# Kernel tuning notes

Measured on AMD Instinct MI355X. Metric: run time of the kernel, lower is better.

## Reference

```python
import jax, jax.numpy as jnp
import numpy as np

TOPK = 4
EPS = 1e-8  # torch CosineSimilarity eps


def _retrieve(query, memory, k):
    # query: [B,S,D], memory: [N,S,D] -> [B,k,S,D]
    q = query.mean(axis=1)                      # [B,D]
    m = memory.mean(axis=1)                     # [N,D]
    qn = q / jnp.maximum(jnp.linalg.norm(q, axis=-1, keepdims=True), EPS)
    mn = m / jnp.maximum(jnp.linalg.norm(m, axis=-1, keepdims=True), EPS)
    sim = qn @ mn.T                             # [B,N] cosine similarity
    valid = (m.sum(axis=-1) != 0).astype(sim.dtype)[None, :]
    sim = sim * valid
    _, idx = jax.lax.top_k(sim, k)              # [B,k]
    return memory[idx]                          # gather -> [B,k,S,D]


def _generate(rem, ret, rem_w, rem_b, ret_w, ret_b, ew1, eb1, ew2, eb2):
    # rem: [B,S,D], ret: [B,K,S,D]; nn.Linear: y = x @ W.T + b
    r = rem @ rem_w.T + rem_b                   # [B,S,D]
    t = jnp.einsum('bksd,ed->bkse', ret, ret_w) + ret_b  # [B,K,S,D]
    score = jax.nn.softmax(
        jnp.einsum('bd,bkd->bk', r.mean(axis=1), t.mean(axis=2)), axis=1)  # [B,K]
    # stacked experts: Linear -> ReLU -> Linear per expert k
    h = jax.nn.relu(jnp.einsum('bksd,ked->bkse', ret, ew1) + eb1[None, :, None, :])
    eo = jnp.einsum('bkse,kfe->bksf', h, ew2) + eb2[None, :, None, :]  # [B,K,S,D]
    return jnp.einsum('bksd,bk->bsd', eo, score)


def setup_inputs() -> dict:
    key = jax.random.key(0)
    B, S, D, N, K = 64, 32, 512, 4096, TOPK
    ks = jax.random.split(key, 24)
    out = {
        'image': jax.random.normal(ks[0], (B, S, D), jnp.float32),
        'text': jax.random.normal(ks[1], (B, S, D), jnp.float32),
        'm1': jax.random.randint(ks[2], (B, 1), 0, 2).astype(jnp.int32),
        'm2': jax.random.randint(ks[3], (B, 1), 0, 2).astype(jnp.int32),
        'mem_image': jax.random.normal(ks[4], (N, S, D), jnp.float32),
        'mem_text': jax.random.normal(ks[5], (N, S, D), jnp.float32),
    }
    i = 6
    for pfx in ('img', 'txt'):
        out[f'{pfx}_rem_w'] = 0.02 * jax.random.normal(ks[i], (D, D), jnp.float32); i += 1
        out[f'{pfx}_rem_b'] = jnp.zeros((D,), jnp.float32)
        out[f'{pfx}_ret_w'] = 0.02 * jax.random.normal(ks[i], (D, D), jnp.float32); i += 1
        out[f'{pfx}_ret_b'] = jnp.zeros((D,), jnp.float32)
        out[f'{pfx}_ew1'] = 0.02 * jax.random.normal(ks[i], (K, D, D), jnp.float32); i += 1
        out[f'{pfx}_eb1'] = jnp.zeros((K, D), jnp.float32)
        out[f'{pfx}_ew2'] = 0.02 * jax.random.normal(ks[i], (K, D, D), jnp.float32); i += 1
        out[f'{pfx}_eb2'] = jnp.zeros((K, D), jnp.float32)
    return out


def reference(image, text, m1, m2, mem_image, mem_text,
              img_rem_w, img_rem_b, img_ret_w, img_ret_b, img_ew1, img_eb1, img_ew2, img_eb2,
              txt_rem_w, txt_rem_b, txt_ret_w, txt_ret_b, txt_ew1, txt_eb1, txt_ew2, txt_eb2):
    m1e = (m1 == 1)[:, 0]  # image exists
    m2e = (m2 == 1)[:, 0]  # text exists

    # generate missing image from existing text (compute full batch, mask after;
    # identical per-sample math to the subset computation in the original)
    ret_img = _retrieve(text, mem_image, TOPK)
    gen_img = _generate(text, ret_img, img_rem_w, img_rem_b, img_ret_w, img_ret_b,
                        img_ew1, img_eb1, img_ew2, img_eb2)
    gen_image_full = jnp.where(m2e[:, None, None], gen_img, 0.0)
    completed_image = jnp.where(jnp.logical_and(~m1e, m2e)[:, None, None], gen_img, image)

    # generate missing text from existing image
    ret_txt = _retrieve(image, mem_text, TOPK)
    gen_txt = _generate(image, ret_txt, txt_rem_w, txt_rem_b, txt_ret_w, txt_ret_b,
                        txt_ew1, txt_eb1, txt_ew2, txt_eb2)
    gen_text_full = jnp.where(m1e[:, None, None], gen_txt, 0.0)
    completed_text = jnp.where(jnp.logical_and(~m2e, m1e)[:, None, None], gen_txt, text)

    return (completed_image, completed_text, gen_image_full, gen_text_full)
```

## Files before the change

### kernel.cpp

```cpp
#include <hip/hip_runtime.h>
#include <hip/hip_fp16.h>

#define BB 64
#define SS 32
#define DD 512
#define NMEM 4096
#define KTOP 4
#define EPSV 1e-8f

typedef _Float16 f16;
typedef f16 f16x8 __attribute__((ext_vector_type(8)));
typedef f16 f16x4 __attribute__((ext_vector_type(4)));
typedef float f32x4 __attribute__((ext_vector_type(4)));

__global__ void k_wconv(const float* __restrict__ s0, const float* __restrict__ s1,
                        const float* __restrict__ s2, const float* __restrict__ s3,
                        f16* __restrict__ d0, f16* __restrict__ d1,
                        f16* __restrict__ d2, f16* __restrict__ d3) {
    const float* s; f16* d;
    switch (blockIdx.y) {
        case 0: s = s0; d = d0; break;
        case 1: s = s1; d = d1; break;
        case 2: s = s2; d = d2; break;
        default: s = s3; d = d3; break;
    }
    size_t i = ((size_t)blockIdx.x * 256 + threadIdx.x) * 4;
    float4 v = *(const float4*)(s + i);
    f16x4 o;
    o[0] = (f16)v.x; o[1] = (f16)v.y; o[2] = (f16)v.z; o[3] = (f16)v.w;
    *(f16x4*)(d + i) = o;
}

__global__ void k_qmean(const float* __restrict__ image, const float* __restrict__ text,
                        float* __restrict__ qmean, float* __restrict__ qn) {
    int mod = blockIdx.x >> 6;
    int b = blockIdx.x & 63;
    const float* q = (mod == 0) ? text : image;
    int t = threadIdx.x;
    const float* base = q + (size_t)b * SS * DD + t * 2;
    float ax = 0.f, ay = 0.f;
#pragma unroll
    for (int s = 0; s < SS; ++s) {
        float2 v = *(const float2*)(base + (size_t)s * DD);
        ax += v.x; ay += v.y;
    }
    ax *= (1.f / SS); ay *= (1.f / SS);
    float* qm = qmean + ((size_t)mod * BB + b) * DD;
    qm[t * 2] = ax; qm[t * 2 + 1] = ay;
    __shared__ float red[256];
    red[t] = ax * ax + ay * ay;
    __syncthreads();
    for (int off = 128; off > 0; off >>= 1) {
        if (t < off) red[t] += red[t + off];
        __syncthreads();
    }
    __shared__ float s_inv;
    if (t == 0) s_inv = 1.f / fmaxf(sqrtf(red[0]), EPSV);
    __syncthreads();
    float inv = s_inv;
    float* qo = qn + ((size_t)mod * BB + b) * DD;
    qo[t * 2] = ax * inv; qo[t * 2 + 1] = ay * inv;
}

__global__ void k_memmean_sim(const float* __restrict__ mem_image, const float* __restrict__ mem_text,
                              const float* __restrict__ qn, float* __restrict__ mmean,
                              float* __restrict__ sim) {
    int mod = blockIdx.x >> 12;
    int n = blockIdx.x & 4095;
    const float* mem = (mod == 0) ? mem_image : mem_text;
    int t = threadIdx.x;
    int cg = t & 127;
    int half = t >> 7;
    const float* base = mem + (size_t)n * SS * DD + (size_t)half * DD + cg * 4;
    float ax = 0.f, ay = 0.f, az = 0.f, aw = 0.f;
#pragma unroll
    for (int i = 0; i < SS / 2; ++i) {
        float4 v = *(const float4*)(base + (size_t)(i * 2) * DD);
        ax += v.x; ay += v.y; az += v.z; aw += v.w;
    }
    __shared__ float part[128][4];
    if (half) { part[cg][0] = ax; part[cg][1] = ay; part[cg][2] = az; part[cg][3] = aw; }
    __syncthreads();
    __shared__ float red[128], red2[128];
    __shared__ float smn[512];
    if (!half) {
        const float inv = 1.f / SS;
        ax = (ax + part[cg][0]) * inv;
        ay = (ay + part[cg][1]) * inv;
        az = (az + part[cg][2]) * inv;
        aw = (aw + part[cg][3]) * inv;
        float4 o; o.x = ax; o.y = ay; o.z = az; o.w = aw;
        *(float4*)(mmean + ((size_t)mod * NMEM + n) * DD + cg * 4) = o;
        red[cg] = ax * ax + ay * ay + az * az + aw * aw;
        red2[cg] = ax + ay + az + aw;
    }
    __syncthreads();
    for (int off = 64; off > 0; off >>= 1) {
        if (t < off) { red[t] += red[t + off]; red2[t] += red2[t + off]; }
        __syncthreads();
    }
    __shared__ float s_scale;
    if (t == 0) {
        float norm = sqrtf(red[0]);
        float valid = (red2[0] != 0.f) ? 1.f : 0.f;
        s_scale = valid / fmaxf(norm, EPSV);
    }
    __syncthreads();
    if (!half) {
        float sc = s_scale;
        smn[cg * 4] = ax * sc; smn[cg * 4 + 1] = ay * sc;
        smn[cg * 4 + 2] = az * sc; smn[cg * 4 + 3] = aw * sc;
    }
    __syncthreads();

    int w = t >> 6, lane = t & 63;
    float4 m0 = *(const float4*)(&smn[lane * 8]);
    float4 m1v = *(const float4*)(&smn[lane * 8 + 4]);
    for (int b = w; b < BB; b += 4) {
        const float* qp = qn + ((size_t)mod * BB + b) * DD + lane * 8;
        float4 q0 = *(const float4*)qp;
        float4 q1 = *(const float4*)(qp + 4);
        float d = m0.x * q0.x + m0.y * q0.y + m0.z * q0.z + m0.w * q0.w
                + m1v.x * q1.x + m1v.y * q1.y + m1v.z * q1.z + m1v.w * q1.w;
#pragma unroll
        for (int o = 32; o > 0; o >>= 1) d += __shfl_down(d, o);
        if (lane == 0) sim[((size_t)mod * BB + b) * NMEM + n] = d;
    }
}

__global__ void k_topk(const float* __restrict__ sim, int* __restrict__ topk) {
    int mod = blockIdx.x >> 6;
    int b = blockIdx.x & 63;
    int lane = threadIdx.x;
    const float* sp = sim + ((size_t)mod * BB + b) * NMEM;
    float tv[4] = {-1e30f, -1e30f, -1e30f, -1e30f};
    int ti[4] = {2147483647, 2147483647, 2147483647, 2147483647};
    for (int i = 0; i < NMEM / 64; ++i) {
        int n = i * 64 + lane;
        float v = sp[n];
        if (v > tv[3]) {
            int p = 3;
            while (p > 0 && v > tv[p - 1]) { tv[p] = tv[p - 1]; ti[p] = ti[p - 1]; --p; }
            tv[p] = v; ti[p] = n;
        }
    }
    __shared__ float cv[256];
    __shared__ int ci[256];
#pragma unroll
    for (int j = 0; j < 4; ++j) { cv[lane * 4 + j] = tv[j]; ci[lane * 4 + j] = ti[j]; }
    __syncthreads();
    if (lane == 0) {
        int* out = topk + (mod * BB + b) * KTOP;
        for (int k = 0; k < KTOP; ++k) {
            float bv = -1e30f; int bi = 2147483647; int bj = -1;
            for (int j = 0; j < 256; ++j) {
                if (cv[j] > bv || (cv[j] == bv && ci[j] < bi)) { bv = cv[j]; bi = ci[j]; bj = j; }
            }
            out[k] = bi;
            cv[bj] = -1e30f; ci[bj] = 2147483647;
        }
    }
}

__global__ void k_score(const float* __restrict__ qmean, const float* __restrict__ mmean,
                        const int* __restrict__ topk,
                        const float* __restrict__ irw, const float* __restrict__ irb,
                        const float* __restrict__ itw, const float* __restrict__ itb,
                        const float* __restrict__ trw, const float* __restrict__ trb,
                        const float* __restrict__ ttw, const float* __restrict__ ttb,
                        float* __restrict__ score) {
    int mod = blockIdx.x >> 6;
    int b = blockIdx.x & 63;
    const float* rem_w = mod ? trw : irw;
    const float* rem_b = mod ? trb : irb;
    const float* ret_w = mod ? ttw : itw;
    const float* ret_b = mod ? ttb : itb;
    __shared__ float x0[512];
    __shared__ float x1[4][512];
    __shared__ float accs[4][4];
    int t = threadIdx.x, w = t >> 6, lane = t & 63;
    const int* idx = topk + (mod * BB + b) * KTOP;
    int i0 = idx[0], i1 = idx[1], i2 = idx[2], i3 = idx[3];
    const float* q = qmean + ((size_t)mod * BB + b) * DD;
    const float* p0 = mmean + ((size_t)mod * NMEM + i0) * DD;
    const float* p1 = mmean + ((size_t)mod * NMEM + i1) * DD;
    const float* p2 = mmean + ((size_t)mod * NMEM + i2) * DD;
    const float* p3 = mmean + ((size_t)mod * NMEM + i3) * DD;
    for (int d0 = t; d0 < DD; d0 += 256) {
        x0[d0] = q[d0];
        x1[0][d0] = p0[d0]; x1[1][d0] = p1[d0]; x1[2][d0] = p2[d0]; x1[3][d0] = p3[d0];
    }
    __syncthreads();
    float sk[4] = {0.f, 0.f, 0.f, 0.f};
    float4 qa = *(const float4*)(&x0[lane * 8]);
    float4 qb = *(const float4*)(&x0[lane * 8 + 4]);
    for (int e = w; e < DD; e += 4) {
        const float* wr = rem_w + (size_t)e * DD + lane * 8;
        const float* tr = ret_w + (size_t)e * DD + lane * 8;
        float4 wa = *(const float4*)wr, wb = *(const float4*)(wr + 4);
        float4 ta = *(const float4*)tr, tb = *(const float4*)(tr + 4);
        float pr = wa.x * qa.x + wa.y * qa.y + wa.z * qa.z + wa.w * qa.w
                 + wb.x * qb.x + wb.y * qb.y + wb.z * qb.z + wb.w * qb.w;
#pragma unroll
        for (int o = 1; o < 64; o <<= 1) pr += __shfl_xor(pr, o);
        float re = pr + rem_b[e];
#pragma unroll
        for (int k = 0; k < 4; ++k) {
            float4 xa = *(const float4*)(&x1[k][lane * 8]);
            float4 xb = *(const float4*)(&x1[k][lane * 8 + 4]);
            float pt = ta.x * xa.x + ta.y * xa.y + ta.z * xa.z + ta.w * xa.w
                     + tb.x * xb.x + tb.y * xb.y + tb.z * xb.z + tb.w * xb.w;
#pragma unroll
            for (int o = 1; o < 64; o <<= 1) pt += __shfl_xor(pt, o);
            sk[k] += re * (pt + ret_b[e]);
        }
    }
    if (lane == 0) { accs[w][0] = sk[0]; accs[w][1] = sk[1]; accs[w][2] = sk[2]; accs[w][3] = sk[3]; }
    __syncthreads();
    if (t == 0) {
        float s[4];
        for (int k = 0; k < 4; ++k) s[k] = accs[0][k] + accs[1][k] + accs[2][k] + accs[3][k];
        float mx = fmaxf(fmaxf(s[0], s[1]), fmaxf(s[2], s[3]));
        float ex[4], sum = 0.f;
        for (int k = 0; k < 4; ++k) { ex[k] = expf(s[k] - mx); sum += ex[k]; }
        for (int k = 0; k < 4; ++k) score[(mod * BB + b) * KTOP + k] = ex[k] / sum;
    }
}

__launch_bounds__(256)
__global__ void k_layer1(const float* __restrict__ mem_image, const float* __restrict__ mem_text,
                         const int* __restrict__ topk, const f16* __restrict__ ew1h,
                         const float* __restrict__ eb1_img, const float* __restrict__ eb1_txt,
                         f16* __restrict__ H) {
    int bx = blockIdx.x, by = blockIdx.y, mk = blockIdx.z;
    int mod = mk >> 2, k = mk & 3;
    const float* mem = (mod == 0) ? mem_image : mem_text;
    const float* eb1 = (mod == 0) ? eb1_img : eb1_txt;

    __shared__ f16 As[64][40];
    __shared__ f16 Bs[64][40];

    int t = threadIdx.x;
    int lrow = t >> 2;
    int lcol = (t & 3) * 8;
    int rg = by * 64 + lrow;
    int bb = rg >> 5, ss = rg & 31;
    int mrow = topk[(mod * BB + bb) * KTOP + k];
    const float* aptr = mem + ((size_t)mrow * SS + ss) * DD + lcol;
    const f16* bptr = ew1h + ((size_t)mk * DD + bx * 64 + lrow) * DD + lcol;

    int w = t >> 6, lane = t & 63;
    int wm = (w >> 1) * 32, wn = (w & 1) * 32;
    int quad = lane >> 4, l16 = lane & 15;

    f32x4 acc[2][2] = {};
    for (int kk = 0; kk < DD; kk += 32) {
        float4 a0 = *(const float4*)(aptr + kk);
        float4 a1 = *(const float4*)(aptr + kk + 4);
        f16x8 bv = *(const f16x8*)(bptr + kk);
        f16x8 af;
        af[0] = (f16)a0.x; af[1] = (f16)a0.y; af[2] = (f16)a0.z; af[3] = (f16)a0.w;
        af[4] = (f16)a1.x; af[5] = (f16)a1.y; af[6] = (f16)a1.z; af[7] = (f16)a1.w;
        *(f16x8*)(&As[lrow][lcol]) = af;
        *(f16x8*)(&Bs[lrow][lcol]) = bv;
        __syncthreads();
#pragma unroll
        for (int tm = 0; tm < 2; ++tm) {
            f16x8 a = *(const f16x8*)(&As[wm + tm * 16 + l16][quad * 8]);
#pragma unroll
            for (int tn = 0; tn < 2; ++tn) {
                f16x8 bf = *(const f16x8*)(&Bs[wn + tn * 16 + l16][quad * 8]);
                acc[tm][tn] = __builtin_amdgcn_mfma_f32_16x16x32_f16(a, bf, acc[tm][tn], 0, 0, 0);
            }
        }
        __syncthreads();
    }
#pragma unroll
    for (int tm = 0; tm < 2; ++tm)
#pragma unroll
        for (int tn = 0; tn < 2; ++tn) {
            int colg = bx * 64 + wn + tn * 16 + l16;
            float bias = eb1[k * DD + colg];
#pragma unroll
            for (int r = 0; r < 4; ++r) {
                int rowg = by * 64 + wm + tm * 16 + quad * 4 + r;
                float v = fmaxf(acc[tm][tn][r] + bias, 0.f);
                H[((size_t)mk * 2048 + rowg) * DD + colg] = (f16)v;
            }
        }
}

__launch_bounds__(256)
__global__ void k_layer2(const f16* __restrict__ H, const f16* __restrict__ ew2h,
                         const float* __restrict__ eb2_img, const float* __restrict__ eb2_txt,
                         const float* __restrict__ score,
                         const float* __restrict__ image, const float* __restrict__ text,
                         const int* __restrict__ m1, const int* __restrict__ m2,
                         float* __restrict__ out) {
    int bx = blockIdx.x, by = blockIdx.y, mod = blockIdx.z;
    __shared__ f16 As[64][40];
    __shared__ f16 Bs[64][40];
    __shared__ float s_sc[2][4];
    int t = threadIdx.x;
    if (t < 8) {
        int bl = t >> 2, kq = t & 3;
        s_sc[bl][kq] = score[(mod * BB + by * 2 + bl) * KTOP + kq];
    }
    int lrow = t >> 2, lcol = (t & 3) * 8;
    int w = t >> 6, lane = t & 63;
    int wm = (w >> 1) * 32, wn = (w & 1) * 32;
    int quad = lane >> 4, l16 = lane & 15;

    float fin[2][2][4] = {};
    for (int k = 0; k < 4; ++k) {
        f32x4 acc[2][2] = {};
        const f16* aptr = H + ((size_t)(mod * 4 + k) * 2048 + by * 64 + lrow) * DD + lcol;
        const f16* bptr = ew2h + ((size_t)(mod * 4 + k) * DD + bx * 64 + lrow) * DD + lcol;
        for (int kk = 0; kk < DD; kk += 32) {
            *(f16x8*)(&As[lrow][lcol]) = *(const f16x8*)(aptr + kk);
            *(f16x8*)(&Bs[lrow][lcol]) = *(const f16x8*)(bptr + kk);
            __syncthreads();
#pragma unroll
            for (int tm = 0; tm < 2; ++tm) {
                f16x8 a = *(const f16x8*)(&As[wm + tm * 16 + l16][quad * 8]);
#pragma unroll
                for (int tn = 0; tn < 2; ++tn) {
                    f16x8 bf = *(const f16x8*)(&Bs[wn + tn * 16 + l16][quad * 8]);
                    acc[tm][tn] = __builtin_amdgcn_mfma_f32_16x16x32_f16(a, bf, acc[tm][tn], 0, 0, 0);
                }
            }
            __syncthreads();
        }
#pragma unroll
        for (int tm = 0; tm < 2; ++tm)
#pragma unroll
            for (int tn = 0; tn < 2; ++tn)
#pragma unroll
                for (int r = 0; r < 4; ++r) {
                    int rloc = wm + tm * 16 + quad * 4 + r;
                    fin[tm][tn][r] += s_sc[rloc >> 5][k] * acc[tm][tn][r];
                }
    }

    const float* eb2 = (mod == 0) ? eb2_img : eb2_txt;
    const float* orig = (mod == 0) ? image : text;
    float* out_comp = out + (size_t)mod * 1048576;
    float* out_gen = out + (size_t)(2 + mod) * 1048576;
#pragma unroll
    for (int tm = 0; tm < 2; ++tm)
#pragma unroll
        for (int tn = 0; tn < 2; ++tn) {
            int colg = bx * 64 + wn + tn * 16 + l16;
#pragma unroll
            for (int r = 0; r < 4; ++r) {
                int rowg = by * 64 + wm + tm * 16 + quad * 4 + r;
                int bl = (rowg >> 5) & 1;
                float g = fin[tm][tn][r];
                for (int k = 0; k < 4; ++k) g += s_sc[bl][k] * eb2[k * DD + colg];
                int bb = rowg >> 5;
                bool e1 = (m1[bb] == 1), e2 = (m2[bb] == 1);
                size_t off = (size_t)rowg * DD + colg;
                if (mod == 0) {
                    out_comp[off] = (!e1 && e2) ? g : orig[off];
                    out_gen[off] = e2 ? g : 0.f;
                } else {
                    out_comp[off] = (!e2 && e1) ? g : orig[off];
                    out_gen[off] = e1 ? g : 0.f;
                }
            }
        }
}

extern "C" void kernel_launch(void* const* d_in, const int* in_sizes, int n_in,
                              void* d_out, int out_size, void* d_ws, size_t ws_size,
                              hipStream_t stream) {
    const float* image = (const float*)d_in[0];
    const float* text = (const float*)d_in[1];
    const int* m1 = (const int*)d_in[2];
    const int* m2 = (const int*)d_in[3];
    const float* mem_image = (const float*)d_in[4];
    const float* mem_text = (const float*)d_in[5];
    const float* i_rem_w = (const float*)d_in[6];
    const float* i_rem_b = (const float*)d_in[7];
    const float* i_ret_w = (const float*)d_in[8];
    const float* i_ret_b = (const float*)d_in[9];
    const float* i_ew1 = (const float*)d_in[10];
    const float* i_eb1 = (const float*)d_in[11];
    const float* i_ew2 = (const float*)d_in[12];
    const float* i_eb2 = (const float*)d_in[13];
    const float* t_rem_w = (const float*)d_in[14];
    const float* t_rem_b = (const float*)d_in[15];
    const float* t_ret_w = (const float*)d_in[16];
    const float* t_ret_b = (const float*)d_in[17];
    const float* t_ew1 = (const float*)d_in[18];
    const float* t_eb1 = (const float*)d_in[19];
    const float* t_ew2 = (const float*)d_in[20];
    const float* t_eb2 = (const float*)d_in[21];

    char* ws = (char*)d_ws;
    float* qmean = (float*)(ws + 0);
    float* qn = (float*)(ws + 262144);
    float* mmean = (float*)(ws + 524288);
    float* sim = (float*)(ws + 17301504);
    int* topk = (int*)(ws + 19398656);
    float* score = (float*)(ws + 19400704);
    f16* ew1h = (f16*)(ws + 19402752);
    f16* ew2h = (f16*)(ws + 23597056);
    f16* H = (f16*)(ws + 27791360);

    k_wconv<<<dim3(1024, 4), 256, 0, stream>>>(i_ew1, t_ew1, i_ew2, t_ew2,
                                               ew1h, ew1h + 1048576, ew2h, ew2h + 1048576);
    k_qmean<<<128, 256, 0, stream>>>(image, text, qmean, qn);
    k_memmean_sim<<<8192, 256, 0, stream>>>(mem_image, mem_text, qn, mmean, sim);
    k_topk<<<128, 64, 0, stream>>>(sim, topk);
    k_score<<<128, 256, 0, stream>>>(qmean, mmean, topk,
                                     i_rem_w, i_rem_b, i_ret_w, i_ret_b,
                                     t_rem_w, t_rem_b, t_ret_w, t_ret_b, score);
    k_layer1<<<dim3(8, 32, 8), 256, 0, stream>>>(mem_image, mem_text, topk, ew1h,
                                                 i_eb1, t_eb1, H);
    k_layer2<<<dim3(8, 32, 2), 256, 0, stream>>>(H, ew2h, i_eb2, t_eb2, score,
                                                 image, text, m1, m2, (float*)d_out);
}
```

Baseline: 906.7 us.

## Split memory-mean from similarity into tiled GEMM; deepen K tiles in expert GEMMs

The fused memmean+similarity kernel is split in two. k_memmean computes row means and a per-row scale factor, using wave shuffles for its reductions. A new tiled fp32 GEMM, k_sim, computes sim with reuse through swizzled shared memory, so qn is no longer re-read from global memory by every memory-row block. Layer1 and layer2 MFMA GEMMs use larger K tiles (64 and 128) to cut the number of barriers per loop, at the cost of more shared memory and an extra kernel launch.

```diff
diff --git a/kernel.cpp b/kernel.cpp
--- a/kernel.cpp
+++ b/kernel.cpp
@@ -62,9 +62,8 @@
     qo[t * 2] = ax * inv; qo[t * 2 + 1] = ay * inv;
 }
 
-__global__ void k_memmean_sim(const float* __restrict__ mem_image, const float* __restrict__ mem_text,
-                              const float* __restrict__ qn, float* __restrict__ mmean,
-                              float* __restrict__ sim) {
+__global__ void k_memmean(const float* __restrict__ mem_image, const float* __restrict__ mem_text,
+                          float* __restrict__ mmean, float* __restrict__ scale) {
     int mod = blockIdx.x >> 12;
     int n = blockIdx.x & 4095;
     const float* mem = (mod == 0) ? mem_image : mem_text;
@@ -79,10 +78,12 @@
         ax += v.x; ay += v.y; az += v.z; aw += v.w;
     }
     __shared__ float part[128][4];
-    if (half) { part[cg][0] = ax; part[cg][1] = ay; part[cg][2] = az; part[cg][3] = aw; }
-    __syncthreads();
-    __shared__ float red[128], red2[128];
-    __shared__ float smn[512];
+    if (half) {
+        float4 p; p.x = ax; p.y = ay; p.z = az; p.w = aw;
+        *(float4*)(&part[cg][0]) = p;
+    }
+    __syncthreads();
+    float sq = 0.f, sv = 0.f;
     if (!half) {
         const float inv = 1.f / SS;
         ax = (ax + part[cg][0]) * inv;
@@ -91,40 +92,81 @@
         aw = (aw + part[cg][3]) * inv;
         float4 o; o.x = ax; o.y = ay; o.z = az; o.w = aw;
         *(float4*)(mmean + ((size_t)mod * NMEM + n) * DD + cg * 4) = o;
-        red[cg] = ax * ax + ay * ay + az * az + aw * aw;
-        red2[cg] = ax + ay + az + aw;
-    }
-    __syncthreads();
-    for (int off = 64; off > 0; off >>= 1) {
-        if (t < off) { red[t] += red[t + off]; red2[t] += red2[t + off]; }
+        sq = ax * ax + ay * ay + az * az + aw * aw;
+        sv = ax + ay + az + aw;
+    }
+    if (t < 128) {
+#pragma unroll
+        for (int o = 32; o > 0; o >>= 1) {
+            sq += __shfl_down(sq, o);
+            sv += __shfl_down(sv, o);
+        }
+    }
+    __shared__ float pq[2], pv[2];
+    if (t < 128 && (t & 63) == 0) { pq[t >> 6] = sq; pv[t >> 6] = sv; }
+    __syncthreads();
+    if (t == 0) {
+        float norm = sqrtf(pq[0] + pq[1]);
+        float valid = ((pv[0] + pv[1]) != 0.f) ? 1.f : 0.f;
+        scale[mod * NMEM + n] = valid / fmaxf(norm, EPSV);
+    }
+}
+
+__global__ void k_sim(const float* __restrict__ qn, const float* __restrict__ mmean,
+                      const float* __restrict__ scale, float* __restrict__ sim) {
+    int nt = blockIdx.x, mod = blockIdx.y;
+    int n0 = nt * 64;
+    __shared__ float As[64][72];
+    __shared__ float Bt[64][68];
+    int t = threadIdx.x;
+    int tb = t >> 4;
+    int tn = t & 15;
+    int swr = (tb & 3) << 2;
+    float acc[4][4] = {};
+    int lr = t >> 2;
+    int lq = (t & 3) * 16;
+    const float* apb = qn + ((size_t)mod * BB + lr) * DD + lq;
+    const float* bpb = mmean + ((size_t)mod * NMEM + n0 + lr) * DD + lq;
+    int swl = ((lr >> 2) & 3) << 2;
+    for (int kk = 0; kk < DD; kk += 64) {
+#pragma unroll
+        for (int j = 0; j < 4; ++j) {
+            float4 v = *(const float4*)(apb + kk + j * 4);
+            int scol = (lq + j * 4) ^ swl;
+            *(float4*)(&As[lr][scol]) = v;
+        }
+#pragma unroll
+        for (int j = 0; j < 4; ++j) {
+            float4 v = *(const float4*)(bpb + kk + j * 4);
+            int kc = lq + j * 4;
+            Bt[kc][lr] = v.x; Bt[kc + 1][lr] = v.y; Bt[kc + 2][lr] = v.z; Bt[kc + 3][lr] = v.w;
+        }
         __syncthreads();
-    }
-    __shared__ float s_scale;
-    if (t == 0) {
-        float norm = sqrtf(red[0]);
-        float valid = (red2[0] != 0.f) ? 1.f : 0.f;
-        s_scale = valid / fmaxf(norm, EPSV);
-    }
-    __syncthreads();
-    if (!half) {
-        float sc = s_scale;
-        smn[cg * 4] = ax * sc; smn[cg * 4 + 1] = ay * sc;
-        smn[cg * 4 + 2] = az * sc; smn[cg * 4 + 3] = aw * sc;
-    }
-    __syncthreads();
-
-    int w = t >> 6, lane = t & 63;
-    float4 m0 = *(const float4*)(&smn[lane * 8]);
-    float4 m1v = *(const float4*)(&smn[lane * 8 + 4]);
-    for (int b = w; b < BB; b += 4) {
-        const float* qp = qn + ((size_t)mod * BB + b) * DD + lane * 8;
-        float4 q0 = *(const float4*)qp;
-        float4 q1 = *(const float4*)(qp + 4);
-        float d = m0.x * q0.x + m0.y * q0.y + m0.z * q0.z + m0.w * q0.w
-                + m1v.x * q1.x + m1v.y * q1.y + m1v.z * q1.z + m1v.w * q1.w;
-#pragma unroll
-        for (int o = 32; o > 0; o >>= 1) d += __shfl_down(d, o);
-        if (lane == 0) sim[((size_t)mod * BB + b) * NMEM + n] = d;
+#pragma unroll
+        for (int k4 = 0; k4 < 64; k4 += 4) {
+            f32x4 av[4], bv[4];
+#pragma unroll
+            for (int r = 0; r < 4; ++r)
+                av[r] = *(const f32x4*)(&As[tb * 4 + r][k4 ^ swr]);
+#pragma unroll
+            for (int j = 0; j < 4; ++j)
+                bv[j] = *(const f32x4*)(&Bt[k4 + j][tn * 4]);
+#pragma unroll
+            for (int r = 0; r < 4; ++r)
+#pragma unroll
+                for (int c = 0; c < 4; ++c)
+                    acc[r][c] += av[r][0] * bv[0][c] + av[r][1] * bv[1][c]
+                               + av[r][2] * bv[2][c] + av[r][3] * bv[3][c];
+        }
+        __syncthreads();
+    }
+    f32x4 sc = *(const f32x4*)(scale + mod * NMEM + n0 + tn * 4);
+#pragma unroll
+    for (int r = 0; r < 4; ++r) {
+        f32x4 o;
+#pragma unroll
+        for (int c = 0; c < 4; ++c) o[c] = acc[r][c] * sc[c];
+        *(f32x4*)(sim + ((size_t)mod * BB + tb * 4 + r) * NMEM + n0 + tn * 4) = o;
     }
 }
 
@@ -237,12 +279,12 @@
     const float* mem = (mod == 0) ? mem_image : mem_text;
     const float* eb1 = (mod == 0) ? eb1_img : eb1_txt;
 
-    __shared__ f16 As[64][40];
-    __shared__ f16 Bs[64][40];
+    __shared__ f16 As[64][72];
+    __shared__ f16 Bs[64][72];
 
     int t = threadIdx.x;
     int lrow = t >> 2;
-    int lcol = (t & 3) * 8;
+    int lcol = (t & 3) * 16;
     int rg = by * 64 + lrow;
     int bb = rg >> 5, ss = rg & 31;
     int mrow = topk[(mod * BB + bb) * KTOP + k];
@@ -254,25 +296,34 @@
     int quad = lane >> 4, l16 = lane & 15;
 
     f32x4 acc[2][2] = {};
-    for (int kk = 0; kk < DD; kk += 32) {
+    for (int kk = 0; kk < DD; kk += 64) {
         float4 a0 = *(const float4*)(aptr + kk);
         float4 a1 = *(const float4*)(aptr + kk + 4);
-        f16x8 bv = *(const f16x8*)(bptr + kk);
-        f16x8 af;
-        af[0] = (f16)a0.x; af[1] = (f16)a0.y; af[2] = (f16)a0.z; af[3] = (f16)a0.w;
-        af[4] = (f16)a1.x; af[5] = (f16)a1.y; af[6] = (f16)a1.z; af[7] = (f16)a1.w;
-        *(f16x8*)(&As[lrow][lcol]) = af;
-        *(f16x8*)(&Bs[lrow][lcol]) = bv;
+        float4 a2 = *(const float4*)(aptr + kk + 8);
+        float4 a3 = *(const float4*)(aptr + kk + 12);
+        f16x8 b0 = *(const f16x8*)(bptr + kk);
+        f16x8 b1 = *(const f16x8*)(bptr + kk + 8);
+        f16x8 af0, af1;
+        af0[0] = (f16)a0.x; af0[1] = (f16)a0.y; af0[2] = (f16)a0.z; af0[3] = (f16)a0.w;
+        af0[4] = (f16)a1.x; af0[5] = (f16)a1.y; af0[6] = (f16)a1.z; af0[7] = (f16)a1.w;
+        af1[0] = (f16)a2.x; af1[1] = (f16)a2.y; af1[2] = (f16)a2.z; af1[3] = (f16)a2.w;
+        af1[4] = (f16)a3.x; af1[5] = (f16)a3.y; af1[6] = (f16)a3.z; af1[7] = (f16)a3.w;
+        *(f16x8*)(&As[lrow][lcol]) = af0;
+        *(f16x8*)(&As[lrow][lcol + 8]) = af1;
+        *(f16x8*)(&Bs[lrow][lcol]) = b0;
+        *(f16x8*)(&Bs[lrow][lcol + 8]) = b1;
         __syncthreads();
 #pragma unroll
-        for (int tm = 0; tm < 2; ++tm) {
-            f16x8 a = *(const f16x8*)(&As[wm + tm * 16 + l16][quad * 8]);
-#pragma unroll
-            for (int tn = 0; tn < 2; ++tn) {
-                f16x8 bf = *(const f16x8*)(&Bs[wn + tn * 16 + l16][quad * 8]);
-                acc[tm][tn] = __builtin_amdgcn_mfma_f32_16x16x32_f16(a, bf, acc[tm][tn], 0, 0, 0);
+        for (int kq = 0; kq < 2; ++kq)
+#pragma unroll
+            for (int tm = 0; tm < 2; ++tm) {
+                f16x8 a = *(const f16x8*)(&As[wm + tm * 16 + l16][kq * 32 + quad * 8]);
+#pragma unroll
+                for (int tn = 0; tn < 2; ++tn) {
+                    f16x8 bf = *(const f16x8*)(&Bs[wn + tn * 16 + l16][kq * 32 + quad * 8]);
+                    acc[tm][tn] = __builtin_amdgcn_mfma_f32_16x16x32_f16(a, bf, acc[tm][tn], 0, 0, 0);
+                }
             }
-        }
         __syncthreads();
     }
 #pragma unroll
@@ -298,15 +349,15 @@
                          const int* __restrict__ m1, const int* __restrict__ m2,
                          float* __restrict__ out) {
     int bx = blockIdx.x, by = blockIdx.y, mod = blockIdx.z;
-    __shared__ f16 As[64][40];
-    __shared__ f16 Bs[64][40];
+    __shared__ f16 As[64][136];
+    __shared__ f16 Bs[64][136];
     __shared__ float s_sc[2][4];
     int t = threadIdx.x;
     if (t < 8) {
         int bl = t >> 2, kq = t & 3;
         s_sc[bl][kq] = score[(mod * BB + by * 2 + bl) * KTOP + kq];
     }
-    int lrow = t >> 2, lcol = (t & 3) * 8;
+    int lrow = t >> 2, lcol = (t & 3) * 32;
     int w = t >> 6, lane = t & 63;
     int wm = (w >> 1) * 32, wn = (w & 1) * 32;
     int quad = lane >> 4, l16 = lane & 15;
@@ -316,19 +367,24 @@
         f32x4 acc[2][2] = {};
         const f16* aptr = H + ((size_t)(mod * 4 + k) * 2048 + by * 64 + lrow) * DD + lcol;
         const f16* bptr = ew2h + ((size_t)(mod * 4 + k) * DD + bx * 64 + lrow) * DD + lcol;
-        for (int kk = 0; kk < DD; kk += 32) {
-            *(f16x8*)(&As[lrow][lcol]) = *(const f16x8*)(aptr + kk);
-            *(f16x8*)(&Bs[lrow][lcol]) = *(const f16x8*)(bptr + kk);
+        for (int kk = 0; kk < DD; kk += 128) {
+#pragma unroll
+            for (int j = 0; j < 4; ++j) {
+                *(f16x8*)(&As[lrow][lcol + j * 8]) = *(const f16x8*)(aptr + kk + j * 8);
+                *(f16x8*)(&Bs[lrow][lcol + j * 8]) = *(const f16x8*)(bptr + kk + j * 8);
+            }
             __syncthreads();
 #pragma unroll
-            for (int tm = 0; tm < 2; ++tm) {
-                f16x8 a = *(const f16x8*)(&As[wm + tm * 16 + l16][quad * 8]);
-#pragma unroll
-                for (int tn = 0; tn < 2; ++tn) {
-                    f16x8 bf = *(const f16x8*)(&Bs[wn + tn * 16 + l16][quad * 8]);
-                    acc[tm][tn] = __builtin_amdgcn_mfma_f32_16x16x32_f16(a, bf, acc[tm][tn], 0, 0, 0);
+            for (int kq = 0; kq < 4; ++kq)
+#pragma unroll
+                for (int tm = 0; tm < 2; ++tm) {
+                    f16x8 a = *(const f16x8*)(&As[wm + tm * 16 + l16][kq * 32 + quad * 8]);
+#pragma unroll
+                    for (int tn = 0; tn < 2; ++tn) {
+                        f16x8 bf = *(const f16x8*)(&Bs[wn + tn * 16 + l16][kq * 32 + quad * 8]);
+                        acc[tm][tn] = __builtin_amdgcn_mfma_f32_16x16x32_f16(a, bf, acc[tm][tn], 0, 0, 0);
+                    }
                 }
-            }
             __syncthreads();
         }
 #pragma unroll
@@ -407,11 +463,13 @@
     f16* ew1h = (f16*)(ws + 19402752);
     f16* ew2h = (f16*)(ws + 23597056);
     f16* H = (f16*)(ws + 27791360);
+    float* scale = (float*)(ws + 44568576);
 
     k_wconv<<<dim3(1024, 4), 256, 0, stream>>>(i_ew1, t_ew1, i_ew2, t_ew2,
                                                ew1h, ew1h + 1048576, ew2h, ew2h + 1048576);
     k_qmean<<<128, 256, 0, stream>>>(image, text, qmean, qn);
-    k_memmean_sim<<<8192, 256, 0, stream>>>(mem_image, mem_text, qn, mmean, sim);
+    k_memmean<<<8192, 256, 0, stream>>>(mem_image, mem_text, mmean, scale);
+    k_sim<<<dim3(64, 2), 256, 0, stream>>>(qn, mmean, scale, sim);
     k_topk<<<128, 64, 0, stream>>>(sim, topk);
     k_score<<<128, 256, 0, stream>>>(qmean, mmean, topk,
                                      i_rem_w, i_rem_b, i_ret_w, i_ret_b,
```

Measured after the change: 1.049 ms. 15.7% more time.
